# Kernel optimization log

Measured on AMD Instinct MI355X. Metric: run time of the kernel, lower is better.

## Reference

```python
import jax, jax.numpy as jnp
import numpy as np

POOL = 7
IMAGE_SHAPE = (1024, 1024, 3)


def _crop_and_resize(fmap, boxes, pool):
    """TF-style crop_and_resize with extrapolation_value=0.
    fmap: [C, H, W]; boxes: [N, (y1,x1,y2,x2)] normalized. Returns [N, C, pool, pool]."""
    C, H, W = fmap.shape
    dt = fmap.dtype
    y1, x1, y2, x2 = boxes[:, 0], boxes[:, 1], boxes[:, 2], boxes[:, 3]
    g = jnp.arange(pool, dtype=dt) / (pool - 1)  # [P] in [0,1]
    ys = (y1[:, None] + g[None, :] * (y2 - y1)[:, None]) * (H - 1)  # [N,P]
    xs = (x1[:, None] + g[None, :] * (x2 - x1)[:, None]) * (W - 1)  # [N,P]
    y0f = jnp.floor(ys); x0f = jnp.floor(xs)
    ly = (ys - y0f).astype(dt); lx = (xs - x0f).astype(dt)
    y0 = jnp.clip(y0f.astype(jnp.int32), 0, H - 1)
    y1i = jnp.clip(y0 + 1, 0, H - 1)
    x0 = jnp.clip(x0f.astype(jnp.int32), 0, W - 1)
    x1i = jnp.clip(x0 + 1, 0, W - 1)
    vy = ((ys >= 0) & (ys <= H - 1)).astype(dt)  # extrapolation_value = 0 outside
    vx = ((xs >= 0) & (xs <= W - 1)).astype(dt)

    def at(yi, xi):
        # gather -> [C, N, P, P]
        return fmap[:, yi[:, :, None], xi[:, None, :]]

    wy0 = (1 - ly)[None, :, :, None]; wy1 = ly[None, :, :, None]
    wx0 = (1 - lx)[None, :, None, :]; wx1 = lx[None, :, None, :]
    val = (at(y0, x0) * wy0 + at(y1i, x0) * wy1) * wx0 \
        + (at(y0, x1i) * wy0 + at(y1i, x1i) * wy1) * wx1
    val = val * (vy[None, :, :, None] * vx[None, :, None, :])
    return jnp.transpose(val, (1, 0, 2, 3))  # [N, C, P, P]


def reference(boxes, p2, p3, p4, p5):
    """pyramid_roi_align: route each box to FPN level 2..5 via the 224-scale
    log2 heuristic, then CropAndResize(pool, pool, 0) from that level.
    Output order matches input box order (original sorts back by box_to_level)."""
    h = boxes[:, 2] - boxes[:, 0]
    w = boxes[:, 3] - boxes[:, 1]
    image_area = float(IMAGE_SHAPE[0] * IMAGE_SHAPE[1])
    roi_level = 4.0 + jnp.log2(jnp.sqrt(h * w) / (224.0 / np.sqrt(image_area)))
    roi_level = jnp.clip(jnp.round(roi_level).astype(jnp.int32), 2, 5)
    boxes_d = jax.lax.stop_gradient(boxes)  # level_boxes.detach() in original
    fmaps = [p2, p3, p4, p5]
    pooled = jnp.zeros((boxes.shape[0], p2.shape[0], POOL, POOL), dtype=p2.dtype)
    for i, level in enumerate(range(2, 6)):
        mask = (roi_level == level).astype(p2.dtype)[:, None, None, None]
        pooled = pooled + mask * _crop_and_resize(fmaps[i], boxes_d, POOL)
    return pooled


def setup_inputs():
    key = jax.random.key(0)
    kb, ks, k2, k3, k4, k5 = jax.random.split(key, 6)
    N, C = 1000, 256
    size = jax.random.uniform(ks, (N, 2), minval=0.02, maxval=0.9)
    tl = jax.random.uniform(kb, (N, 2)) * (1.0 - size)  # top-left so box stays in [0,1]
    boxes = jnp.concatenate([tl[:, 0:1], tl[:, 1:2],
                             tl[:, 0:1] + size[:, 0:1], tl[:, 1:2] + size[:, 1:2]], axis=1)
    p2 = jax.random.normal(k2, (C, 256, 256), jnp.float32)
    p3 = jax.random.normal(k3, (C, 128, 128), jnp.float32)
    p4 = jax.random.normal(k4, (C, 64, 64), jnp.float32)
    p5 = jax.random.normal(k5, (C, 32, 32), jnp.float32)
    return {"boxes": boxes, "p2": p2, "p3": p3, "p4": p4, "p5": p5}
```

## Files before the change

kernel.cpp:

```cpp
#include <hip/hip_runtime.h>


#define POOL 7
#define NCH  256
#define ELEMS_PER_BOX (NCH * POOL * POOL)
#define QCH 64
#define WCH 16
#define SCH 4
#define NSTEPS 4
#define ROWS 14
#define SLOTS 512
#define CG 8
#define NGROUPS 8
#define GROUP_OUT (CG * 49)

typedef float f2 __attribute__((ext_vector_type(2)));
typedef __attribute__((address_space(1))) const void* gas_ptr;
typedef __attribute__((address_space(3))) void*       las_ptr;

__global__ __launch_bounds__(256, 4) void roi_align_kernel(
    const float* __restrict__ boxes,
    const float* __restrict__ p2, const float* __restrict__ p3,
    const float* __restrict__ p4, const float* __restrict__ p5,
    float* __restrict__ out, int N)
{
    const int bid     = blockIdx.x;
    const int n       = bid >> 2;
    const int quarter = bid & 3;

    __shared__ float s_stage[4][SLOTS * 4];
    __shared__ float s_a[49], s_b[49], s_w0[49], s_w1[49];
    __shared__ int   s_dx[49];
    __shared__ int   s_off0[49], s_off1[49];
    __shared__ int   s_rowoff[ROWS];
    __shared__ int   s_HW, s_xb0, s_s4s, s_fast;
    __shared__ const float* s_fmap;

    const int tid = threadIdx.x;

    if (tid < 49) {
        const float by1 = boxes[4 * n + 0];
        const float bx1 = boxes[4 * n + 1];
        const float by2 = boxes[4 * n + 2];
        const float bx2 = boxes[4 * n + 3];
        const float h = by2 - by1;
        const float w = bx2 - bx1;
        float rl = 4.0f + log2f(sqrtf(h * w) / 0.21875f);
        int level = (int)rintf(rl);
        level = min(5, max(2, level));
        const int H = 256 >> (level - 2);
        const int W = H;
        const int py = tid / 7;
        const int px = tid - 7 * py;

        const float ty = (float)py / 6.0f;
        const float ys = (by1 + ty * (by2 - by1)) * (float)(H - 1);
        const float yf = floorf(ys);
        const float ly = ys - yf;
        int y0 = (int)yf; y0 = min(H - 1, max(0, y0));
        const int y1 = min(H - 1, y0 + 1);
        const float vy = (ys >= 0.0f && ys <= (float)(H - 1)) ? 1.0f : 0.0f;

        const float tx = (float)px / 6.0f;
        const float xs = (bx1 + tx * (bx2 - bx1)) * (float)(W - 1);
        const float xf = floorf(xs);
        const float lx = xs - xf;
        int x0 = (int)xf; x0 = min(W - 1, max(0, x0));
        const float vx = (xs >= 0.0f && xs <= (float)(W - 1)) ? 1.0f : 0.0f;
        const int xb = min(x0, W - 2);
        const bool edge = (x0 != xb);
        const float a = edge ? 0.0f : vx * (1.0f - lx);
        const float b = edge ? vx : vx * lx;

        const float xsA = bx1 * (float)(W - 1);
        int xA = (int)floorf(xsA); xA = min(W - 1, max(0, xA));
        const int xbA = min(xA, W - 2);
        const float xsB = bx2 * (float)(W - 1);
        int xB = (int)floorf(xsB); xB = min(W - 1, max(0, xB));
        const int xbB = min(xB, W - 2);
        const int xb0  = xbA & ~3;
        const int need = xbB + 2 - xb0;
        const int sa4  = (need + 3) >> 2;

        s_off0[tid] = y0 * W + xb;
        s_off1[tid] = y1 * W + xb;
        s_a[tid] = a;
        s_b[tid] = b;
        s_w0[tid] = vy * (1.0f - ly);
        s_w1[tid] = vy * ly;
        s_dx[tid] = xb - xb0;
        if (px == 0) {
            s_rowoff[2 * py]     = y0 * W;
            s_rowoff[2 * py + 1] = y1 * W;
        }
        if (tid == 0) {
            s_HW   = H * W;
            s_fmap = (level == 2) ? p2 : (level == 3) ? p3 : (level == 4) ? p4 : p5;
            s_xb0  = xb0;
            s_s4s  = sa4 | 1;
            s_fast = (need <= 32) ? 1 : 0;
        }
    }
    __syncthreads();

    const int HW = s_HW;
    const float* __restrict__ lvl = s_fmap;
    const int lane = tid & 63;
    const int wave = tid >> 6;

    if (s_fast) {
        const int s4s = s_s4s;
        const int S   = 4 * s4s;
        const int nslots = 56 * s4s;
        const unsigned lim = (unsigned)(NCH * HW - 4);
        float* const slice = s_stage[wave];
        const int chbase = quarter * QCH + wave * WCH;
        const unsigned cb0 = (unsigned)chbase * (unsigned)HW;

        unsigned inv0, inv1, inv2, inv3, inv4, inv5, inv6, inv7;
#define SLOTMETA(k, bvar)                                                     \
        { const int idx = (k) * 64 + lane;                                    \
          if (idx < nslots) {                                                 \
              const int rid = idx / s4s;               \
              const int q   = idx - rid * s4s;         \
              const int cl  = rid / 14;                \
              const int r   = rid - 14 * cl;           \
              bvar = (unsigned)(cl * HW + s_rowoff[r] + s_xb0 + 4 * q);       \
          } else bvar = 0x40000000u; }
        SLOTMETA(0, inv0) SLOTMETA(1, inv1) SLOTMETA(2, inv2) SLOTMETA(3, inv3)
        SLOTMETA(4, inv4) SLOTMETA(5, inv5) SLOTMETA(6, inv6) SLOTMETA(7, inv7)
#undef SLOTMETA

        bool  act0, act1, act2_, act3;
        int   to0, to1, to2, to3;
        float aa0, bb0, w00, w10, aa1, bb1, w01, w11;
        float aa2, bb2, w02, w12, aa3, bb3, w03, w13;
#define CELLMETA(j, act, to, aa, bb, w0v, w1v)                                \
        { const int oidx = (j) * 64 + lane;                                   \
          act = (oidx < SCH * 49);                                            \
          const int oc = min(oidx, SCH * 49 - 1);                             \
          const int cc = oc / 49;                                             \
          const int pp = oc - 49 * cc;                                        \
          to  = (cc * ROWS + 2 * (pp / 7)) * S + s_dx[pp];                    \
          aa = s_a[pp]; bb = s_b[pp]; w0v = s_w0[pp]; w1v = s_w1[pp]; }
        CELLMETA(0, act0, to0, aa0, bb0, w00, w10)
        CELLMETA(1, act1, to1, aa1, bb1, w01, w11)
        CELLMETA(2, act2_, to2, aa2, bb2, w02, w12)
        CELLMETA(3, act3, to3, aa3, bb3, w03, w13)
#undef CELLMETA

        float* __restrict__ opw =
            out + (size_t)n * ELEMS_PER_BOX + (size_t)chbase * 49;

        for (int s = 0; s < NSTEPS; ++s) {
            const unsigned stepoff = cb0 + (unsigned)(s * SCH * HW);
#define GLD(k, bvar)                                                          \
            if ((k) * 64 < nslots) {                                          \
                const unsigned o = min(stepoff + bvar, lim);                  \
                __builtin_amdgcn_global_load_lds((gas_ptr)(lvl + o),          \
                    (las_ptr)(slice + ((k) * 64 + lane) * 4), 16, 0, 0);      \
            }
            GLD(0, inv0) GLD(1, inv1) GLD(2, inv2) GLD(3, inv3)
            GLD(4, inv4) GLD(5, inv5) GLD(6, inv6) GLD(7, inv7)
#undef GLD
            asm volatile("s_waitcnt vmcnt(0)" ::: "memory");
            __builtin_amdgcn_sched_barrier(0);

            float* __restrict__ o_s = opw + s * (SCH * 49);
#define CELL(j, act, to, aa, bb, w0v, w1v)                                    \
            if (act) {                                                        \
                const float t00 = slice[(to)],     t01 = slice[(to) + 1];     \
                const float t10 = slice[(to) + S], t11 = slice[(to) + S + 1]; \
                o_s[(j) * 64 + lane] =                                        \
                    (t00 * aa + t01 * bb) * w0v + (t10 * aa + t11 * bb) * w1v;\
            }
            CELL(0, act0, to0, aa0, bb0, w00, w10)
            CELL(1, act1, to1, aa1, bb1, w01, w11)
            CELL(2, act2_, to2, aa2, bb2, w02, w12)
            CELL(3, act3, to3, aa3, bb3, w03, w13)
#undef CELL
            __builtin_amdgcn_sched_barrier(0);
            asm volatile("" ::: "memory");
        }
    } else {
        const int c1  = tid / 49,  p1  = tid - 49 * c1;
        const int o2  = 256 + tid;
        const int c2  = o2 / 49,   p2i = o2 - 49 * c2;
        const bool act2 = (tid < GROUP_OUT - 256);

        const float a1 = s_a[p1],  b1 = s_b[p1],  w01f = s_w0[p1],  w11f = s_w1[p1];
        const float a2 = s_a[p2i], b2 = s_b[p2i], w02f = s_w0[p2i], w12f = s_w1[p2i];
        const int off01 = s_off0[p1],  off11 = s_off1[p1];
        const int off02 = s_off0[p2i], off12 = s_off1[p2i];

        const float* __restrict__ fbase = lvl + (size_t)(quarter * QCH) * HW;
        float* __restrict__ op =
            out + (size_t)n * ELEMS_PER_BOX + quarter * (QCH * 49);
        for (int g = 0; g < NGROUPS; ++g) {
            const float* pl1 = fbase + (size_t)(g * CG + c1) * HW;
            const f2 q0 = *(const f2*)(pl1 + off01);
            const f2 q1 = *(const f2*)(pl1 + off11);
            const float r0 = q0.x * a1 + q0.y * b1;
            const float r1 = q1.x * a1 + q1.y * b1;
            op[g * GROUP_OUT + tid] = r0 * w01f + r1 * w11f;
            if (act2) {
                const float* pl2 = fbase + (size_t)(g * CG + c2) * HW;
                const f2 u0 = *(const f2*)(pl2 + off02);
                const f2 u1 = *(const f2*)(pl2 + off12);
                const float s0 = u0.x * a2 + u0.y * b2;
                const float s1 = u1.x * a2 + u1.y * b2;
                op[g * GROUP_OUT + 256 + tid] = s0 * w02f + s1 * w12f;
            }
        }
    }
}

extern "C" void kernel_launch(void* const* d_in, const int* in_sizes, int n_in,
                              void* d_out, int out_size, void* d_ws, size_t ws_size,
                              hipStream_t stream) {
    const float* boxes = (const float*)d_in[0];
    const float* p2    = (const float*)d_in[1];
    const float* p3    = (const float*)d_in[2];
    const float* p4    = (const float*)d_in[3];
    const float* p5    = (const float*)d_in[4];
    float* out = (float*)d_out;
    const int N = in_sizes[0] / 4;

    roi_align_kernel<<<N * 4, 256, 0, stream>>>(boxes, p2, p3, p4, p5, out, N);
}
```

Measured before the change: 147.6 us.

## Double-buffer LDS staging with templated slot counts and smaller blocks

The fast path now splits each box into eighths using 128-thread blocks (2 waves), and double-buffers global_load_lds staging per wave. Loads for the next step are issued while the current buffer is being interpolated, using partial vmcnt waits. The slot count per row is made a compile-time template parameter, which removes runtime division and unused load slots. Output stores are deferred to the end, and the fast-path threshold drops from a need of 32 to 28 to fit the smaller buffers. The intent is to hide load latency and raise parallelism, at the cost of more registers, more blocks, and more boxes falling back to the slow path.

New measurement: 145.1 us. Within noise of the previous version (-1.7%).

```diff
diff --git a/kernel.cpp b/kernel.cpp
--- a/kernel.cpp
+++ b/kernel.cpp
@@ -4,36 +4,168 @@
 #define POOL 7
 #define NCH  256
 #define ELEMS_PER_BOX (NCH * POOL * POOL)
-#define QCH 64
+#define ECH 32
 #define WCH 16
 #define SCH 4
 #define NSTEPS 4
 #define ROWS 14
-#define SLOTS 512
-#define CG 8
-#define NGROUPS 8
-#define GROUP_OUT (CG * 49)
+#define MAXG 7
+#define BUFSLOT (MAXG * 64)
+#define STEPOUT (SCH * 49)
 
 typedef float f2 __attribute__((ext_vector_type(2)));
 typedef __attribute__((address_space(1))) const void* gas_ptr;
 typedef __attribute__((address_space(3))) void*       las_ptr;
 
-__global__ __launch_bounds__(256, 4) void roi_align_kernel(
+#define VMWAIT(n) asm volatile("s_waitcnt vmcnt(" #n ")" ::: "memory")
+
+template<int S4S>
+__device__ __forceinline__ void fast_steps(
+    const float* __restrict__ lvl, float* __restrict__ opw,
+    float* __restrict__ buf0, float* __restrict__ buf1,
+    const int lane, const int HW, const unsigned cb0, const unsigned lim,
+    const int xb0, const int* s_rowoff, const int* s_dx,
+    const float* s_a, const float* s_b, const float* s_w0, const float* s_w1)
+{
+    constexpr int G   = (56 * S4S + 63) / 64;
+    constexpr int S   = 4 * S4S;
+    constexpr int NSL = 56 * S4S;
+
+    unsigned inv0 = 0x40000000u, inv1 = 0x40000000u, inv2 = 0x40000000u,
+             inv3 = 0x40000000u, inv4 = 0x40000000u, inv5 = 0x40000000u,
+             inv6 = 0x40000000u;
+#define SLOTMETA(k, var)                                                      \
+    if constexpr ((k) < G) {                                                  \
+        const int idx = (k) * 64 + lane;                                      \
+        if (idx < NSL) {                                                      \
+            const int rid = idx / S4S;                         \
+            const int q   = idx - rid * S4S;                                  \
+            const int cl  = rid / 14;                                         \
+            const int r   = rid - 14 * cl;                                    \
+            var = (unsigned)(cl * HW + s_rowoff[r] + xb0 + 4 * q);            \
+        }                                                                     \
+    }
+    SLOTMETA(0, inv0) SLOTMETA(1, inv1) SLOTMETA(2, inv2) SLOTMETA(3, inv3)
+    SLOTMETA(4, inv4) SLOTMETA(5, inv5) SLOTMETA(6, inv6)
+#undef SLOTMETA
+
+    int   to0, to1, to2, to3;
+    float aa0, bb0, w00, w10, aa1, bb1, w01, w11;
+    float aa2, bb2, w02, w12, aa3, bb3, w03, w13;
+#define CELLMETA(j, tov, aav, bbv, w0v, w1v)                                  \
+    { int oidx = (j) * 64 + lane;                                             \
+      oidx = oidx < STEPOUT ? oidx : STEPOUT - 1;                             \
+      const int cc = oidx / 49;                                               \
+      const int pp = oidx - 49 * cc;                                          \
+      tov = (cc * ROWS + 2 * (pp / 7)) * S + s_dx[pp];                        \
+      aav = s_a[pp]; bbv = s_b[pp]; w0v = s_w0[pp]; w1v = s_w1[pp]; }
+    CELLMETA(0, to0, aa0, bb0, w00, w10)
+    CELLMETA(1, to1, aa1, bb1, w01, w11)
+    CELLMETA(2, to2, aa2, bb2, w02, w12)
+    CELLMETA(3, to3, aa3, bb3, w03, w13)
+#undef CELLMETA
+
+#define GLD1(k, var, so, bp)                                                  \
+    if constexpr ((k) < G) {                                                  \
+        unsigned o_ = (so) + var; o_ = o_ > lim ? lim : o_;                   \
+        __builtin_amdgcn_global_load_lds((gas_ptr)(lvl + o_),                 \
+            (las_ptr)((bp) + ((k) * 64 + lane) * 4), 16, 0, 0);               \
+    }
+#define ISSUE(t, bp)                                                          \
+    { const unsigned so_ = cb0 + (unsigned)((t) * SCH * HW);                  \
+      GLD1(0, inv0, so_, bp) GLD1(1, inv1, so_, bp) GLD1(2, inv2, so_, bp)    \
+      GLD1(3, inv3, so_, bp) GLD1(4, inv4, so_, bp) GLD1(5, inv5, so_, bp)    \
+      GLD1(6, inv6, so_, bp) }
+#define CELLC(bp, tov, aav, bbv, w0v, w1v, rvar)                              \
+    { const float t00 = (bp)[tov],     t01 = (bp)[tov + 1];                   \
+      const float t10 = (bp)[tov + S], t11 = (bp)[tov + S + 1];               \
+      rvar = (t00 * aav + t01 * bbv) * w0v + (t10 * aav + t11 * bbv) * w1v; }
+#define VMWAIT_G                                                              \
+    if constexpr (G == 1) { VMWAIT(1); }                                      \
+    else if constexpr (G == 3) { VMWAIT(3); }                                 \
+    else if constexpr (G == 5) { VMWAIT(5); }                                 \
+    else { VMWAIT(7); }
+
+    float r00, r01, r02, r03, r10, r11, r12, r13;
+    float r20, r21, r22, r23, r30, r31, r32, r33;
+
+    ISSUE(0, buf0)
+    ISSUE(1, buf1)
+
+    VMWAIT_G;
+    __builtin_amdgcn_sched_barrier(0);
+    CELLC(buf0, to0, aa0, bb0, w00, w10, r00)
+    CELLC(buf0, to1, aa1, bb1, w01, w11, r01)
+    CELLC(buf0, to2, aa2, bb2, w02, w12, r02)
+    CELLC(buf0, to3, aa3, bb3, w03, w13, r03)
+    asm volatile("s_waitcnt lgkmcnt(0)" ::: "memory");
+    __builtin_amdgcn_sched_barrier(0);
+    ISSUE(2, buf0)
+
+    VMWAIT_G;
+    __builtin_amdgcn_sched_barrier(0);
+    CELLC(buf1, to0, aa0, bb0, w00, w10, r10)
+    CELLC(buf1, to1, aa1, bb1, w01, w11, r11)
+    CELLC(buf1, to2, aa2, bb2, w02, w12, r12)
+    CELLC(buf1, to3, aa3, bb3, w03, w13, r13)
+    asm volatile("s_waitcnt lgkmcnt(0)" ::: "memory");
+    __builtin_amdgcn_sched_barrier(0);
+    ISSUE(3, buf1)
+
+    VMWAIT_G;
+    __builtin_amdgcn_sched_barrier(0);
+    CELLC(buf0, to0, aa0, bb0, w00, w10, r20)
+    CELLC(buf0, to1, aa1, bb1, w01, w11, r21)
+    CELLC(buf0, to2, aa2, bb2, w02, w12, r22)
+    CELLC(buf0, to3, aa3, bb3, w03, w13, r23)
+
+    VMWAIT(0);
+    __builtin_amdgcn_sched_barrier(0);
+    CELLC(buf1, to0, aa0, bb0, w00, w10, r30)
+    CELLC(buf1, to1, aa1, bb1, w01, w11, r31)
+    CELLC(buf1, to2, aa2, bb2, w02, w12, r32)
+    CELLC(buf1, to3, aa3, bb3, w03, w13, r33)
+
+    const bool tail = (lane < STEPOUT - 192);
+    opw[0 * STEPOUT +   0 + lane] = r00;
+    opw[0 * STEPOUT +  64 + lane] = r01;
+    opw[0 * STEPOUT + 128 + lane] = r02;
+    if (tail) opw[0 * STEPOUT + 192 + lane] = r03;
+    opw[1 * STEPOUT +   0 + lane] = r10;
+    opw[1 * STEPOUT +  64 + lane] = r11;
+    opw[1 * STEPOUT + 128 + lane] = r12;
+    if (tail) opw[1 * STEPOUT + 192 + lane] = r13;
+    opw[2 * STEPOUT +   0 + lane] = r20;
+    opw[2 * STEPOUT +  64 + lane] = r21;
+    opw[2 * STEPOUT + 128 + lane] = r22;
+    if (tail) opw[2 * STEPOUT + 192 + lane] = r23;
+    opw[3 * STEPOUT +   0 + lane] = r30;
+    opw[3 * STEPOUT +  64 + lane] = r31;
+    opw[3 * STEPOUT + 128 + lane] = r32;
+    if (tail) opw[3 * STEPOUT + 192 + lane] = r33;
+
+#undef GLD1
+#undef ISSUE
+#undef CELLC
+#undef VMWAIT_G
+}
+
+__global__ __launch_bounds__(128, 4) void roi_align_kernel(
     const float* __restrict__ boxes,
     const float* __restrict__ p2, const float* __restrict__ p3,
     const float* __restrict__ p4, const float* __restrict__ p5,
     float* __restrict__ out, int N)
 {
-    const int bid     = blockIdx.x;
-    const int n       = bid >> 2;
-    const int quarter = bid & 3;
-
-    __shared__ float s_stage[4][SLOTS * 4];
+    const int bid    = blockIdx.x;
+    const int n      = bid >> 3;
+    const int eighth = bid & 7;
+
+    __shared__ float s_stage[2][2][BUFSLOT * 4];
     __shared__ float s_a[49], s_b[49], s_w0[49], s_w1[49];
     __shared__ int   s_dx[49];
     __shared__ int   s_off0[49], s_off1[49];
     __shared__ int   s_rowoff[ROWS];
-    __shared__ int   s_HW, s_xb0, s_s4s, s_fast;
+    __shared__ int   s_HW, s_xb0, s_sel;
     __shared__ const float* s_fmap;
 
     const int tid = threadIdx.x;
@@ -97,8 +229,7 @@
             s_HW   = H * W;
             s_fmap = (level == 2) ? p2 : (level == 3) ? p3 : (level == 4) ? p4 : p5;
             s_xb0  = xb0;
-            s_s4s  = sa4 | 1;
-            s_fast = (need <= 32) ? 1 : 0;
+            s_sel  = (need <= 28) ? (sa4 | 1) : 0;
         }
     }
     __syncthreads();
@@ -107,109 +238,58 @@
     const float* __restrict__ lvl = s_fmap;
     const int lane = tid & 63;
     const int wave = tid >> 6;
-
-    if (s_fast) {
-        const int s4s = s_s4s;
-        const int S   = 4 * s4s;
-        const int nslots = 56 * s4s;
+    const int sel  = s_sel;
+
+    if (sel) {
+        const int chw = eighth * ECH + wave * WCH;
+        const unsigned cb0 = (unsigned)chw * (unsigned)HW;
         const unsigned lim = (unsigned)(NCH * HW - 4);
-        float* const slice = s_stage[wave];
-        const int chbase = quarter * QCH + wave * WCH;
-        const unsigned cb0 = (unsigned)chbase * (unsigned)HW;
-
-        unsigned inv0, inv1, inv2, inv3, inv4, inv5, inv6, inv7;
-#define SLOTMETA(k, bvar)                                                     \
-        { const int idx = (k) * 64 + lane;                                    \
-          if (idx < nslots) {                                                 \
-              const int rid = idx / s4s;               \
-              const int q   = idx - rid * s4s;         \
-              const int cl  = rid / 14;                \
-              const int r   = rid - 14 * cl;           \
-              bvar = (unsigned)(cl * HW + s_rowoff[r] + s_xb0 + 4 * q);       \
-          } else bvar = 0x40000000u; }
-        SLOTMETA(0, inv0) SLOTMETA(1, inv1) SLOTMETA(2, inv2) SLOTMETA(3, inv3)
-        SLOTMETA(4, inv4) SLOTMETA(5, inv5) SLOTMETA(6, inv6) SLOTMETA(7, inv7)
-#undef SLOTMETA
-
-        bool  act0, act1, act2_, act3;
-        int   to0, to1, to2, to3;
-        float aa0, bb0, w00, w10, aa1, bb1, w01, w11;
-        float aa2, bb2, w02, w12, aa3, bb3, w03, w13;
-#define CELLMETA(j, act, to, aa, bb, w0v, w1v)                                \
-        { const int oidx = (j) * 64 + lane;                                   \
-          act = (oidx < SCH * 49);                                            \
-          const int oc = min(oidx, SCH * 49 - 1);                             \
-          const int cc = oc / 49;                                             \
-          const int pp = oc - 49 * cc;                                        \
-          to  = (cc * ROWS + 2 * (pp / 7)) * S + s_dx[pp];                    \
-          aa = s_a[pp]; bb = s_b[pp]; w0v = s_w0[pp]; w1v = s_w1[pp]; }
-        CELLMETA(0, act0, to0, aa0, bb0, w00, w10)
-        CELLMETA(1, act1, to1, aa1, bb1, w01, w11)
-        CELLMETA(2, act2_, to2, aa2, bb2, w02, w12)
-        CELLMETA(3, act3, to3, aa3, bb3, w03, w13)
-#undef CELLMETA
-
+        float* buf0 = &s_stage[wave][0][0];
+        float* buf1 = &s_stage[wave][1][0];
         float* __restrict__ opw =
-            out + (size_t)n * ELEMS_PER_BOX + (size_t)chbase * 49;
-
-        for (int s = 0; s < NSTEPS; ++s) {
-            const unsigned stepoff = cb0 + (unsigned)(s * SCH * HW);
-#define GLD(k, bvar)                                                          \
-            if ((k) * 64 < nslots) {                                          \
-                const unsigned o = min(stepoff + bvar, lim);                  \
-                __builtin_amdgcn_global_load_lds((gas_ptr)(lvl + o),          \
-                    (las_ptr)(slice + ((k) * 64 + lane) * 4), 16, 0, 0);      \
-            }
-            GLD(0, inv0) GLD(1, inv1) GLD(2, inv2) GLD(3, inv3)
-            GLD(4, inv4) GLD(5, inv5) GLD(6, inv6) GLD(7, inv7)
-#undef GLD
-            asm volatile("s_waitcnt vmcnt(0)" ::: "memory");
-            __builtin_amdgcn_sched_barrier(0);
-
-            float* __restrict__ o_s = opw + s * (SCH * 49);
-#define CELL(j, act, to, aa, bb, w0v, w1v)                                    \
-            if (act) {                                                        \
-                const float t00 = slice[(to)],     t01 = slice[(to) + 1];     \
-                const float t10 = slice[(to) + S], t11 = slice[(to) + S + 1]; \
-                o_s[(j) * 64 + lane] =                                        \
-                    (t00 * aa + t01 * bb) * w0v + (t10 * aa + t11 * bb) * w1v;\
-            }
-            CELL(0, act0, to0, aa0, bb0, w00, w10)
-            CELL(1, act1, to1, aa1, bb1, w01, w11)
-            CELL(2, act2_, to2, aa2, bb2, w02, w12)
-            CELL(3, act3, to3, aa3, bb3, w03, w13)
-#undef CELL
-            __builtin_amdgcn_sched_barrier(0);
-            asm volatile("" ::: "memory");
-        }
+            out + (size_t)n * ELEMS_PER_BOX + (size_t)chw * 49;
+
+        if (sel == 3)
+            fast_steps<3>(lvl, opw, buf0, buf1, lane, HW, cb0, lim, s_xb0,
+                          s_rowoff, s_dx, s_a, s_b, s_w0, s_w1);
+        else if (sel == 5)
+            fast_steps<5>(lvl, opw, buf0, buf1, lane, HW, cb0, lim, s_xb0,
+                          s_rowoff, s_dx, s_a, s_b, s_w0, s_w1);
+        else if (sel == 7)
+            fast_steps<7>(lvl, opw, buf0, buf1, lane, HW, cb0, lim, s_xb0,
+                          s_rowoff, s_dx, s_a, s_b, s_w0, s_w1);
+        else
+            fast_steps<1>(lvl, opw, buf0, buf1, lane, HW, cb0, lim, s_xb0,
+                          s_rowoff, s_dx, s_a, s_b, s_w0, s_w1);
     } else {
         const int c1  = tid / 49,  p1  = tid - 49 * c1;
-        const int o2  = 256 + tid;
-        const int c2  = o2 / 49,   p2i = o2 - 49 * c2;
-        const bool act2 = (tid < GROUP_OUT - 256);
+        const int o2  = 128 + tid;
+        const int o2c = o2 < STEPOUT ? o2 : STEPOUT - 1;
+        const int c2  = o2c / 49,  p2i = o2c - 49 * c2;
+        const bool act2 = (tid < STEPOUT - 128);
 
         const float a1 = s_a[p1],  b1 = s_b[p1],  w01f = s_w0[p1],  w11f = s_w1[p1];
         const float a2 = s_a[p2i], b2 = s_b[p2i], w02f = s_w0[p2i], w12f = s_w1[p2i];
         const int off01 = s_off0[p1],  off11 = s_off1[p1];
         const int off02 = s_off0[p2i], off12 = s_off1[p2i];
 
-        const float* __restrict__ fbase = lvl + (size_t)(quarter * QCH) * HW;
+        const float* __restrict__ fbase = lvl + (size_t)(eighth * ECH) * HW;
         float* __restrict__ op =
-            out + (size_t)n * ELEMS_PER_BOX + quarter * (QCH * 49);
-        for (int g = 0; g < NGROUPS; ++g) {
-            const float* pl1 = fbase + (size_t)(g * CG + c1) * HW;
+            out + (size_t)n * ELEMS_PER_BOX + (size_t)(eighth * ECH) * 49;
+        for (int g = 0; g < 8; ++g) {
+            const float* pl1 = fbase + (size_t)(g * SCH + c1) * HW;
             const f2 q0 = *(const f2*)(pl1 + off01);
             const f2 q1 = *(const f2*)(pl1 + off11);
             const float r0 = q0.x * a1 + q0.y * b1;
             const float r1 = q1.x * a1 + q1.y * b1;
-            op[g * GROUP_OUT + tid] = r0 * w01f + r1 * w11f;
+            op[g * STEPOUT + tid] = r0 * w01f + r1 * w11f;
             if (act2) {
-                const float* pl2 = fbase + (size_t)(g * CG + c2) * HW;
+                const float* pl2 = fbase + (size_t)(g * SCH + c2) * HW;
                 const f2 u0 = *(const f2*)(pl2 + off02);
                 const f2 u1 = *(const f2*)(pl2 + off12);
                 const float s0 = u0.x * a2 + u0.y * b2;
                 const float s1 = u1.x * a2 + u1.y * b2;
-                op[g * GROUP_OUT + 256 + tid] = s0 * w02f + s1 * w12f;
+                op[g * STEPOUT + 128 + tid] = s0 * w02f + s1 * w12f;
             }
         }
     }
@@ -226,5 +306,5 @@
     float* out = (float*)d_out;
     const int N = in_sizes[0] / 4;
 
-    roi_align_kernel<<<N * 4, 256, 0, stream>>>(boxes, p2, p3, p4, p5, out, N);
+    roi_align_kernel<<<N * 8, 128, 0, stream>>>(boxes, p2, p3, p4, p5, out, N);
 }
```
